# Kernel optimization log

Hardware: AMD Instinct MI355X
Metric: run time of the kernel (lower is better)

## Reference

```python
import jax, jax.numpy as jnp
import numpy as np

N_NODES = 50000
N_EDGES = 800000


def _sage_conv(h, ei, W_l, W_r, b_l):
    """PyG SAGEConv: lin_l(mean_{j->i} h_j) + lin_r(h_i). lin_l has bias, lin_r does not."""
    src, dst = ei[0], ei[1]
    # mean-aggregate raw features first (linear commutes with mean) to avoid [E, out] intermediates
    msum = jax.ops.segment_sum(h[src], dst, num_segments=N_NODES)          # [N, d]
    cnt = jax.ops.segment_sum(jnp.ones((ei.shape[1], 1), h.dtype), dst,
                              num_segments=N_NODES)                         # [N, 1]
    mean = msum / jnp.maximum(cnt, 1.0)
    return mean @ W_l + b_l + h @ W_r


def setup_inputs() -> dict:
    key = jax.random.key(0)
    ks = jax.random.split(key, 8)
    d_in, d_hid, d_out = 64, 64, 32
    return {
        "x": jax.random.normal(ks[0], (N_NODES, d_in), dtype=jnp.float32),
        "ei0": jax.random.randint(ks[1], (2, N_EDGES), 0, N_NODES, dtype=jnp.int32),
        "ei1": jax.random.randint(ks[2], (2, N_EDGES), 0, N_NODES, dtype=jnp.int32),
        "Wl": jax.random.normal(ks[3], (2, 2, d_in, d_hid), dtype=jnp.float32) * 0.05,
        "Wr": jax.random.normal(ks[4], (2, 2, d_in, d_hid), dtype=jnp.float32) * 0.05,
        "bl": jax.random.normal(ks[5], (2, 2, d_hid), dtype=jnp.float32) * 0.05,
        "lin_W": jax.random.normal(ks[6], (d_hid, d_out), dtype=jnp.float32) * 0.05,
        "lin_b": jax.random.normal(ks[7], (d_out,), dtype=jnp.float32) * 0.05,
    }


def reference(x, ei0, ei1, Wl, Wr, bl, lin_W, lin_b):
    edge_indices = (ei0, ei1)  # one edge_index per relation
    h = x
    for l in range(2):  # layers (structurally fixed)
        out = None
        for r, ei in enumerate(edge_indices):  # HeteroConv aggr='sum' over relations
            y = _sage_conv(h, ei, Wl[l, r], Wr[l, r], bl[l, r])
            out = y if out is None else out + y
        h = jax.nn.relu(out)
    return h @ lin_W + lin_b
```

## Files before the change

kernel.cpp:

```cpp
#include <hip/hip_runtime.h>

#define NN 50000
#define CAP 32
#define OVF_CAP 4096
#define SHARD_W 64
#define NSH 782
#define NPB 512

__device__ __forceinline__ unsigned short f2bf(float f) {
    unsigned u = __float_as_uint(f);
    u += 0x7fffu + ((u >> 16) & 1u);
    return (unsigned short)(u >> 16);
}
__device__ __forceinline__ float bf2f(unsigned short u) {
    return __uint_as_float(((unsigned)u) << 16);
}


__global__ __launch_bounds__(256) void shard_hist(
    const float* __restrict__ x, unsigned short* __restrict__ xb,
    const int* __restrict__ ei0, int E0,
    const int* __restrict__ ei1, int E1,
    unsigned short* __restrict__ hist16,
    int* __restrict__ ovf_cnt)
{
    int gtid = blockIdx.x * 256 + threadIdx.x;
    int gsz  = gridDim.x * 256;
    for (int i = gtid; i < NN * 16; i += gsz) {
        float4 v = ((const float4*)x)[i];
        ushort4 o;
        o.x = f2bf(v.x); o.y = f2bf(v.y); o.z = f2bf(v.z); o.w = f2bf(v.w);
        ((ushort4*)xb)[i] = o;
    }
    if (gtid < 8) ovf_cnt[gtid] = 0;

    __shared__ unsigned lh[NSH];
    int local = blockIdx.x; int rel = 0;
    if (local >= NPB) { local -= NPB; rel = 1; }
    int pb = (local & 7) * (NPB / 8) + (local >> 3);
    const int* ei = rel ? ei1 : ei0;
    int E         = rel ? E1  : E0;
    int ce = (E + NPB - 1) / NPB;
    int lo = pb * ce, hi = min(lo + ce, E);

    for (int i = threadIdx.x; i < NSH; i += 256) lh[i] = 0;
    __syncthreads();
    for (int t = lo + threadIdx.x; t < hi; t += 256)
        atomicAdd(&lh[ei[E + t] >> 6], 1u);
    __syncthreads();
    for (int i = threadIdx.x; i < NSH; i += 256)
        hist16[((size_t)rel * NSH + i) * NPB + pb] = (unsigned short)lh[i];
}

__global__ __launch_bounds__(256) void total_pass(
    const unsigned short* __restrict__ hist16, int* __restrict__ tot)
{
    int gw = (blockIdx.x * 256 + threadIdx.x) >> 6;
    int lane = threadIdx.x & 63;
    if (gw >= 2 * NSH) return;
    uint4 v = ((const uint4*)(hist16 + (size_t)gw * NPB))[lane];
    unsigned s = (v.x & 0xffffu) + (v.x >> 16) + (v.y & 0xffffu) + (v.y >> 16)
               + (v.z & 0xffffu) + (v.z >> 16) + (v.w & 0xffffu) + (v.w >> 16);
    for (int off = 32; off; off >>= 1) s += __shfl_down(s, off);
    if (lane == 0) tot[gw] = (int)s;
}

__global__ __launch_bounds__(256) void scan_pass(
    const int* __restrict__ tot, int* __restrict__ sbase)
{
    __shared__ int ps[256];
    int t = threadIdx.x;
    int v[7];
    int s = 0;
    #pragma unroll
    for (int j = 0; j < 7; j++) {
        int i = t * 7 + j;
        v[j] = (i < 2 * NSH) ? tot[i] : 0;
        s += v[j];
    }
    ps[t] = s;
    __syncthreads();
    for (int off = 1; off < 256; off <<= 1) {
        int add = (t >= off) ? ps[t - off] : 0;
        __syncthreads();
        ps[t] += add;
        __syncthreads();
    }
    int run = (t == 0) ? 0 : ps[t - 1];
    #pragma unroll
    for (int j = 0; j < 7; j++) {
        int i = t * 7 + j;
        if (i < 2 * NSH) sbase[i] = run;
        run += v[j];
    }
    if (t == 255) sbase[2 * NSH] = run;
}

__global__ __launch_bounds__(256) void blockbase_pass(
    const unsigned short* __restrict__ hist16, const int* __restrict__ sbase,
    unsigned* __restrict__ pbase)
{
    int gw = (blockIdx.x * 256 + threadIdx.x) >> 6;
    int lane = threadIdx.x & 63;
    if (gw >= 2 * NSH) return;
    uint4 v = ((const uint4*)(hist16 + (size_t)gw * NPB))[lane];
    unsigned c[8] = {v.x & 0xffffu, v.x >> 16, v.y & 0xffffu, v.y >> 16,
                     v.z & 0xffffu, v.z >> 16, v.w & 0xffffu, v.w >> 16};
    unsigned lsum = 0;
    #pragma unroll
    for (int j = 0; j < 8; j++) lsum += c[j];
    unsigned incl = lsum;
    for (int off = 1; off < 64; off <<= 1) {
        unsigned n = __shfl_up(incl, off);
        if (lane >= off) incl += n;
    }
    unsigned run = (unsigned)sbase[gw] + incl - lsum;
    unsigned* prow = pbase + (size_t)gw * NPB + lane * 8;
    #pragma unroll
    for (int j = 0; j < 8; j++) { prow[j] = run; run += c[j]; }
}

__global__ __launch_bounds__(256) void partition_pass(
    const int* __restrict__ ei0, int E0,
    const int* __restrict__ ei1, int E1,
    const unsigned* __restrict__ pbase,
    unsigned* __restrict__ compact)
{
    __shared__ unsigned lbase[NSH];
    __shared__ unsigned lrank[NSH];
    int local = blockIdx.x; int rel = 0;
    if (local >= NPB) { local -= NPB; rel = 1; }
    int pb = (local & 7) * (NPB / 8) + (local >> 3);
    const int* ei = rel ? ei1 : ei0;
    int E         = rel ? E1  : E0;
    int ce = (E + NPB - 1) / NPB;
    int lo = pb * ce, hi = min(lo + ce, E);

    for (int i = threadIdx.x; i < NSH; i += 256) {
        lbase[i] = pbase[((size_t)rel * NSH + i) * NPB + pb];
        lrank[i] = 0;
    }
    __syncthreads();
    for (int t = lo + threadIdx.x; t < hi; t += 256) {
        int dst = ei[E + t];
        int src = ei[t];
        int s = dst >> 6;
        unsigned r = atomicAdd(&lrank[s], 1u);
        compact[lbase[s] + r] = ((unsigned)dst << 16) | (unsigned)src;
    }
}

__global__ __launch_bounds__(256) void bin_pass(
    const unsigned* __restrict__ compact, const int* __restrict__ sbase,
    unsigned short* __restrict__ bins, int* __restrict__ deg,
    int2* __restrict__ ovf, int* __restrict__ ovf_cnt)
{
    __shared__ unsigned lcnt[SHARD_W];
    int bid = blockIdx.x;
    int rel = bid / NSH;
    int s   = bid - rel * NSH;
    if (threadIdx.x < SHARD_W) lcnt[threadIdx.x] = 0;
    __syncthreads();
    int base = sbase[bid];
    int tot  = sbase[bid + 1] - base;
    int taskbase = rel * NN + s * SHARD_W;
    for (int j = threadIdx.x; j < tot; j += 256) {
        unsigned e = compact[base + j];
        int dst = (int)(e >> 16);
        int src = (int)(e & 0xffffu);
        int loc = dst & (SHARD_W - 1);
        unsigned r = atomicAdd(&lcnt[loc], 1u);
        int task = taskbase + loc;
        if (r < CAP) {
            bins[(size_t)task * CAP + r] = (unsigned short)src;
        } else {
            int o = atomicAdd(ovf_cnt, 1);
            if (o < OVF_CAP) ovf[o] = make_int2(task, src);
        }
    }
    __syncthreads();
    if (threadIdx.x < SHARD_W) {
        int node = s * SHARD_W + threadIdx.x;
        if (node < NN) deg[rel * NN + node] = (int)lcnt[threadIdx.x];
    }
}

__global__ __launch_bounds__(256) void aggregate(
    const unsigned short* __restrict__ bins, const int* __restrict__ deg,
    const unsigned short* __restrict__ hb, unsigned short* __restrict__ agg,
    const int2* __restrict__ ovf, const int* __restrict__ ovf_cnt)
{
    int lane = threadIdx.x & 63;
    int half = lane >> 5;
    int p = lane & 31;
    int wid = (blockIdx.x * blockDim.x + threadIdx.x) >> 6;
    int nwaves = (gridDim.x * blockDim.x) >> 6;
    const unsigned int* hb32 = (const unsigned int*)hb;
    unsigned int* agg32 = (unsigned int*)agg;

    for (int task = wid; task < 2 * NN; task += nwaves) {
        int d = deg[task];
        int m = min(d, CAP);
        int idx = 0;
        if (lane < m) idx = bins[(size_t)task * CAP + lane];
        float a00=0.f,a01=0.f, a10=0.f,a11=0.f, a20=0.f,a21=0.f, a30=0.f,a31=0.f;
        int F = m >> 1;
        int q = 0;
        for (; q + 4 <= F; q += 4) {
            int s0 = __shfl(idx, 2*(q+0) + half);
            int s1 = __shfl(idx, 2*(q+1) + half);
            int s2 = __shfl(idx, 2*(q+2) + half);
            int s3 = __shfl(idx, 2*(q+3) + half);
            unsigned u0 = hb32[(size_t)s0 * 32 + p];
            unsigned u1 = hb32[(size_t)s1 * 32 + p];
            unsigned u2 = hb32[(size_t)s2 * 32 + p];
            unsigned u3 = hb32[(size_t)s3 * 32 + p];
            a00 += __uint_as_float(u0 << 16); a01 += __uint_as_float(u0 & 0xffff0000u);
            a10 += __uint_as_float(u1 << 16); a11 += __uint_as_float(u1 & 0xffff0000u);
            a20 += __uint_as_float(u2 << 16); a21 += __uint_as_float(u2 & 0xffff0000u);
            a30 += __uint_as_float(u3 << 16); a31 += __uint_as_float(u3 & 0xffff0000u);
        }
        for (; q < F; ++q) {
            int s = __shfl(idx, 2*q + half);
            unsigned u = hb32[(size_t)s * 32 + p];
            a00 += __uint_as_float(u << 16); a01 += __uint_as_float(u & 0xffff0000u);
        }
        if (m & 1) {
            int s = __shfl(idx, m - 1);
            if (half == 0) {
                unsigned u = hb32[(size_t)s * 32 + p];
                a00 += __uint_as_float(u << 16); a01 += __uint_as_float(u & 0xffff0000u);
            }
        }
        if (d > CAP) {
            int cnt = min(*ovf_cnt, OVF_CAP);
            for (int e = 0; e < cnt; ++e) {
                int2 v = ovf[e];
                if (v.x == task && half == 0) {
                    unsigned u = hb32[(size_t)v.y * 32 + p];
                    a00 += __uint_as_float(u << 16); a01 += __uint_as_float(u & 0xffff0000u);
                }
            }
        }
        float s0 = (a00 + a10) + (a20 + a30);
        float s1 = (a01 + a11) + (a21 + a31);
        s0 += __shfl_xor(s0, 32);
        s1 += __shfl_xor(s1, 32);
        if (half == 0) {
            float inv = 1.0f / (float)max(d, 1);
            unsigned lo = (unsigned)f2bf(s0 * inv);
            unsigned hi = (unsigned)f2bf(s1 * inv);
            agg32[(size_t)task * 32 + p] = lo | (hi << 16);
        }
    }
}

#define RST 132
__global__ __launch_bounds__(256) void layer_gemm(
    const unsigned short* __restrict__ agg0, const unsigned short* __restrict__ agg1,
    const unsigned short* __restrict__ selfb,
    const float* __restrict__ Wl0, const float* __restrict__ Wl1,
    const float* __restrict__ Wr0, const float* __restrict__ Wr1,
    const float* __restrict__ b0, const float* __restrict__ b1,
    unsigned short* __restrict__ hb16)
{
    __shared__ float Wch[64 * 64];
    __shared__ float rowsT[64 * RST];
    __shared__ float bias[64];

    int tid = threadIdx.x;
    int base = blockIdx.x * 128;
    if (tid < 64) bias[tid] = b0[tid] + b1[tid];

    int j8 = (tid & 7) * 8;
    int n4 = (tid >> 3) * 4;

    float acc[4][8];
    #pragma unroll
    for (int i = 0; i < 4; i++)
        #pragma unroll
        for (int c = 0; c < 8; c++) acc[i][c] = 0.f;

    for (int chunk = 0; chunk < 3; chunk++) {
        const float* W = (chunk == 0) ? Wl0 : (chunk == 1) ? Wl1 : Wr0;
        const unsigned short* src = (chunk == 0) ? agg0 : (chunk == 1) ? agg1 : selfb;
        __syncthreads();
        #pragma unroll
        for (int r = 0; r < 4; r++) {
            int i = tid + 256 * r;
            float4 w = *(const float4*)&W[i * 4];
            if (chunk == 2) {
                float4 w2 = *(const float4*)&Wr1[i * 4];
                w.x += w2.x; w.y += w2.y; w.z += w2.z; w.w += w2.w;
            }
            *(float4*)&Wch[i * 4] = w;
        }
        #pragma unroll
        for (int r = 0; r < 8; r++) {
            int i = tid + 256 * r;
            int node = i >> 4;
            int k4 = (i & 15) * 4;
            int g = base + node;
            ushort4 u = make_ushort4(0, 0, 0, 0);
            if (g < NN) u = *(const ushort4*)&src[(size_t)g * 64 + k4];
            rowsT[(k4 + 0) * RST + node] = bf2f(u.x);
            rowsT[(k4 + 1) * RST + node] = bf2f(u.y);
            rowsT[(k4 + 2) * RST + node] = bf2f(u.z);
            rowsT[(k4 + 3) * RST + node] = bf2f(u.w);
        }
        __syncthreads();
        #pragma unroll 4
        for (int k = 0; k < 64; k++) {
            float4 wa = *(const float4*)&Wch[k * 64 + j8];
            float4 wb = *(const float4*)&Wch[k * 64 + j8 + 4];
            float4 rv = *(const float4*)&rowsT[k * RST + n4];
            float w[8] = {wa.x, wa.y, wa.z, wa.w, wb.x, wb.y, wb.z, wb.w};
            float rr[4] = {rv.x, rv.y, rv.z, rv.w};
            #pragma unroll
            for (int i = 0; i < 4; i++)
                #pragma unroll
                for (int c = 0; c < 8; c++)
                    acc[i][c] = fmaf(rr[i], w[c], acc[i][c]);
        }
    }

    #pragma unroll
    for (int i = 0; i < 4; i++) {
        int g = base + n4 + i;
        if (g < NN) {
            ushort4 p0, p1;
            p0.x = f2bf(fmaxf(acc[i][0] + bias[j8 + 0], 0.f));
            p0.y = f2bf(fmaxf(acc[i][1] + bias[j8 + 1], 0.f));
            p0.z = f2bf(fmaxf(acc[i][2] + bias[j8 + 2], 0.f));
            p0.w = f2bf(fmaxf(acc[i][3] + bias[j8 + 3], 0.f));
            p1.x = f2bf(fmaxf(acc[i][4] + bias[j8 + 4], 0.f));
            p1.y = f2bf(fmaxf(acc[i][5] + bias[j8 + 5], 0.f));
            p1.z = f2bf(fmaxf(acc[i][6] + bias[j8 + 6], 0.f));
            p1.w = f2bf(fmaxf(acc[i][7] + bias[j8 + 7], 0.f));
            *(ushort4*)&hb16[(size_t)g * 64 + j8]     = p0;
            *(ushort4*)&hb16[(size_t)g * 64 + j8 + 4] = p1;
        }
    }
}

__global__ __launch_bounds__(256) void layer_gemm_final(
    const unsigned short* __restrict__ agg0, const unsigned short* __restrict__ agg1,
    const unsigned short* __restrict__ selfb,
    const float* __restrict__ Wl0, const float* __restrict__ Wl1,
    const float* __restrict__ Wr0, const float* __restrict__ Wr1,
    const float* __restrict__ b0, const float* __restrict__ b1,
    const float* __restrict__ linW, const float* __restrict__ linb,
    float* __restrict__ out)
{
    __shared__ float Wch[64 * 64];
    __shared__ float rowsT[64 * RST];
    __shared__ float bias[64];

    int tid = threadIdx.x;
    int base = blockIdx.x * 128;
    if (tid < 64) bias[tid] = b0[tid] + b1[tid];

    int j8 = (tid & 7) * 8;
    int n4 = (tid >> 3) * 4;

    float acc[4][8];
    #pragma unroll
    for (int i = 0; i < 4; i++)
        #pragma unroll
        for (int c = 0; c < 8; c++) acc[i][c] = 0.f;

    for (int chunk = 0; chunk < 3; chunk++) {
        const float* W = (chunk == 0) ? Wl0 : (chunk == 1) ? Wl1 : Wr0;
        const unsigned short* src = (chunk == 0) ? agg0 : (chunk == 1) ? agg1 : selfb;
        __syncthreads();
        #pragma unroll
        for (int r = 0; r < 4; r++) {
            int i = tid + 256 * r;
            float4 w = *(const float4*)&W[i * 4];
            if (chunk == 2) {
                float4 w2 = *(const float4*)&Wr1[i * 4];
                w.x += w2.x; w.y += w2.y; w.z += w2.z; w.w += w2.w;
            }
            *(float4*)&Wch[i * 4] = w;
        }
        #pragma unroll
        for (int r = 0; r < 8; r++) {
            int i = tid + 256 * r;
            int node = i >> 4;
            int k4 = (i & 15) * 4;
            int g = base + node;
            ushort4 u = make_ushort4(0, 0, 0, 0);
            if (g < NN) u = *(const ushort4*)&src[(size_t)g * 64 + k4];
            rowsT[(k4 + 0) * RST + node] = bf2f(u.x);
            rowsT[(k4 + 1) * RST + node] = bf2f(u.y);
            rowsT[(k4 + 2) * RST + node] = bf2f(u.z);
            rowsT[(k4 + 3) * RST + node] = bf2f(u.w);
        }
        __syncthreads();
        #pragma unroll 4
        for (int k = 0; k < 64; k++) {
            float4 wa = *(const float4*)&Wch[k * 64 + j8];
            float4 wb = *(const float4*)&Wch[k * 64 + j8 + 4];
            float4 rv = *(const float4*)&rowsT[k * RST + n4];
            float w[8] = {wa.x, wa.y, wa.z, wa.w, wb.x, wb.y, wb.z, wb.w};
            float rr[4] = {rv.x, rv.y, rv.z, rv.w};
            #pragma unroll
            for (int i = 0; i < 4; i++)
                #pragma unroll
                for (int c = 0; c < 8; c++)
                    acc[i][c] = fmaf(rr[i], w[c], acc[i][c]);
        }
    }

    float o[4][8];
    #pragma unroll
    for (int i = 0; i < 4; i++)
        #pragma unroll
        for (int c = 0; c < 8; c++)
            o[i][c] = fmaxf(acc[i][c] + bias[j8 + c], 0.f);

    __syncthreads();

    #pragma unroll
    for (int r = 0; r < 2; r++) {
        int i = tid + 256 * r;
        *(float4*)&Wch[i * 4] = *(const float4*)&linW[i * 4];
    }
    if (tid < 32) bias[tid] = linb[tid];
    #pragma unroll
    for (int i = 0; i < 4; i++)
        #pragma unroll
        for (int c = 0; c < 8; c++)
            rowsT[(j8 + c) * RST + (n4 + i)] = o[i][c];
    __syncthreads();

    int j4 = (tid & 7) * 4;
    float acc2[4][4];
    #pragma unroll
    for (int i = 0; i < 4; i++)
        #pragma unroll
        for (int c = 0; c < 4; c++) acc2[i][c] = 0.f;
    #pragma unroll 4
    for (int k = 0; k < 64; k++) {
        float4 w = *(const float4*)&Wch[k * 32 + j4];
        float4 rv = *(const float4*)&rowsT[k * RST + n4];
        float wr[4] = {w.x, w.y, w.z, w.w};
        float rr[4] = {rv.x, rv.y, rv.z, rv.w};
        #pragma unroll
        for (int i = 0; i < 4; i++)
            #pragma unroll
            for (int c = 0; c < 4; c++)
                acc2[i][c] = fmaf(rr[i], wr[c], acc2[i][c]);
    }
    #pragma unroll
    for (int i = 0; i < 4; i++) {
        int g = base + n4 + i;
        if (g < NN) {
            float4 ov;
            ov.x = acc2[i][0] + bias[j4 + 0];
            ov.y = acc2[i][1] + bias[j4 + 1];
            ov.z = acc2[i][2] + bias[j4 + 2];
            ov.w = acc2[i][3] + bias[j4 + 3];
            *(float4*)&out[(size_t)g * 32 + j4] = ov;
        }
    }
}

extern "C" void kernel_launch(void* const* d_in, const int* in_sizes, int n_in,
                              void* d_out, int out_size, void* d_ws, size_t ws_size,
                              hipStream_t stream)
{
    const float* x    = (const float*)d_in[0];
    const int*   ei0  = (const int*)d_in[1];
    const int*   ei1  = (const int*)d_in[2];
    const float* Wl   = (const float*)d_in[3];
    const float* Wr   = (const float*)d_in[4];
    const float* bl   = (const float*)d_in[5];
    const float* linW = (const float*)d_in[6];
    const float* linb = (const float*)d_in[7];
    float* out = (float*)d_out;

    int E0 = in_sizes[1] / 2;
    int E1 = in_sizes[2] / 2;

    unsigned short* bins = (unsigned short*)d_ws;
    unsigned short* h1b  = bins + (size_t)2 * NN * CAP;
    unsigned short* aggb = h1b + (size_t)NN * 64;
    unsigned short* agg0 = aggb;
    unsigned short* agg1 = aggb + (size_t)NN * 64;
    unsigned short* xb   = aggb + (size_t)2 * NN * 64;
    int*  deg     = (int*)(xb + (size_t)NN * 64);
    int*  ovf_cnt = deg + 2 * NN;
    int2* ovf     = (int2*)(ovf_cnt + 8);

    unsigned*       compact = (unsigned*)h1b;
    unsigned short* hist16  = aggb;
    unsigned*       pbase   = (unsigned*)(aggb + (size_t)2 * NSH * NPB);
    int*            tot     = (int*)(aggb + (size_t)2 * NSH * NPB * 3);
    int*            sbase   = tot + 2 * NSH;

    dim3 blk(256);
    int ggrid = (NN + 127) / 128;
    int wave_grid = (2 * NSH * 64 + 255) / 256;

    shard_hist<<<2 * NPB, blk, 0, stream>>>(x, xb, ei0, E0, ei1, E1,
                                            hist16, ovf_cnt);
    total_pass<<<wave_grid, blk, 0, stream>>>(hist16, tot);
    scan_pass<<<1, blk, 0, stream>>>(tot, sbase);
    blockbase_pass<<<wave_grid, blk, 0, stream>>>(hist16, sbase, pbase);
    partition_pass<<<2 * NPB, blk, 0, stream>>>(ei0, E0, ei1, E1, pbase, compact);
    bin_pass<<<2 * NSH, blk, 0, stream>>>(compact, sbase, bins, deg, ovf, ovf_cnt);

    aggregate<<<4096, blk, 0, stream>>>(bins, deg, xb, aggb, ovf, ovf_cnt);
    layer_gemm<<<ggrid, blk, 0, stream>>>(agg0, agg1, xb,
        Wl + 0, Wl + 4096, Wr + 0, Wr + 4096, bl + 0, bl + 64, h1b);

    aggregate<<<4096, blk, 0, stream>>>(bins, deg, h1b, aggb, ovf, ovf_cnt);
    layer_gemm_final<<<ggrid, blk, 0, stream>>>(agg0, agg1, h1b,
        Wl + 8192, Wl + 12288, Wr + 8192, Wr + 12288, bl + 128, bl + 192,
        linW, linb, out);
}
```

Baseline: 243.6 us.

## Fuse edge binning into per-shard aggregation using LDS bins

Removes the separate bin_pass kernel and the global bins, deg and overflow arrays. Each aggregation block now bins its shard's compacted edges into shared memory, keeping overflow edges in a local list, then gathers neighbour features for its 64 nodes. This avoids writing and re-reading the global bin arrays and saves a launch. In exchange, binning runs once per layer instead of once overall, and the aggregate grid is fixed at one block per shard, with each wave handling 16 nodes in sequence.

```diff
diff --git a/kernel.cpp b/kernel.cpp
--- a/kernel.cpp
+++ b/kernel.cpp
@@ -2,7 +2,7 @@
 
 #define NN 50000
 #define CAP 32
-#define OVF_CAP 4096
+#define OVF_LDS 1024
 #define SHARD_W 64
 #define NSH 782
 #define NPB 512
@@ -21,8 +21,7 @@
     const float* __restrict__ x, unsigned short* __restrict__ xb,
     const int* __restrict__ ei0, int E0,
     const int* __restrict__ ei1, int E1,
-    unsigned short* __restrict__ hist16,
-    int* __restrict__ ovf_cnt)
+    unsigned short* __restrict__ hist16)
 {
     int gtid = blockIdx.x * 256 + threadIdx.x;
     int gsz  = gridDim.x * 256;
@@ -32,7 +31,6 @@
         o.x = f2bf(v.x); o.y = f2bf(v.y); o.z = f2bf(v.z); o.w = f2bf(v.w);
         ((ushort4*)xb)[i] = o;
     }
-    if (gtid < 8) ovf_cnt[gtid] = 0;
 
     __shared__ unsigned lh[NSH];
     int local = blockIdx.x; int rel = 0;
@@ -150,59 +148,51 @@
     }
 }
 
-__global__ __launch_bounds__(256) void bin_pass(
+__global__ __launch_bounds__(256) void aggregate_shard(
     const unsigned* __restrict__ compact, const int* __restrict__ sbase,
-    unsigned short* __restrict__ bins, int* __restrict__ deg,
-    int2* __restrict__ ovf, int* __restrict__ ovf_cnt)
-{
+    const unsigned short* __restrict__ hb, unsigned short* __restrict__ agg)
+{
+    __shared__ unsigned short lbins[SHARD_W * CAP];
     __shared__ unsigned lcnt[SHARD_W];
+    __shared__ unsigned lovf[OVF_LDS];
+    __shared__ unsigned lovf_cnt;
+
     int bid = blockIdx.x;
     int rel = bid / NSH;
     int s   = bid - rel * NSH;
-    if (threadIdx.x < SHARD_W) lcnt[threadIdx.x] = 0;
-    __syncthreads();
-    int base = sbase[bid];
-    int tot  = sbase[bid + 1] - base;
-    int taskbase = rel * NN + s * SHARD_W;
-    for (int j = threadIdx.x; j < tot; j += 256) {
-        unsigned e = compact[base + j];
-        int dst = (int)(e >> 16);
-        int src = (int)(e & 0xffffu);
-        int loc = dst & (SHARD_W - 1);
-        unsigned r = atomicAdd(&lcnt[loc], 1u);
-        int task = taskbase + loc;
-        if (r < CAP) {
-            bins[(size_t)task * CAP + r] = (unsigned short)src;
-        } else {
-            int o = atomicAdd(ovf_cnt, 1);
-            if (o < OVF_CAP) ovf[o] = make_int2(task, src);
-        }
-    }
-    __syncthreads();
-    if (threadIdx.x < SHARD_W) {
-        int node = s * SHARD_W + threadIdx.x;
-        if (node < NN) deg[rel * NN + node] = (int)lcnt[threadIdx.x];
-    }
-}
-
-__global__ __launch_bounds__(256) void aggregate(
-    const unsigned short* __restrict__ bins, const int* __restrict__ deg,
-    const unsigned short* __restrict__ hb, unsigned short* __restrict__ agg,
-    const int2* __restrict__ ovf, const int* __restrict__ ovf_cnt)
-{
-    int lane = threadIdx.x & 63;
+    int tid = threadIdx.x;
+    int lane = tid & 63;
     int half = lane >> 5;
     int p = lane & 31;
-    int wid = (blockIdx.x * blockDim.x + threadIdx.x) >> 6;
-    int nwaves = (gridDim.x * blockDim.x) >> 6;
-    const unsigned int* hb32 = (const unsigned int*)hb;
-    unsigned int* agg32 = (unsigned int*)agg;
-
-    for (int task = wid; task < 2 * NN; task += nwaves) {
-        int d = deg[task];
+    int wid = tid >> 6;
+
+    if (tid < SHARD_W) lcnt[tid] = 0;
+    if (tid == 0) lovf_cnt = 0;
+    __syncthreads();
+
+    int base = sbase[bid];
+    int tt   = sbase[bid + 1] - base;
+    for (int j = tid; j < tt; j += 256) {
+        unsigned e = compact[base + j];
+        int loc = (int)(e >> 16) & (SHARD_W - 1);
+        unsigned r = atomicAdd(&lcnt[loc], 1u);
+        if (r < CAP) {
+            lbins[loc * CAP + r] = (unsigned short)(e & 0xffffu);
+        } else {
+            unsigned o = atomicAdd(&lovf_cnt, 1u);
+            if (o < OVF_LDS) lovf[o] = ((unsigned)loc << 16) | (e & 0xffffu);
+        }
+    }
+    __syncthreads();
+
+    const unsigned* hb32 = (const unsigned*)hb;
+    unsigned* agg32 = (unsigned*)agg;
+    for (int t = 0; t < 16; ++t) {
+        int loc = wid * 16 + t;
+        int d = (int)lcnt[loc];
         int m = min(d, CAP);
         int idx = 0;
-        if (lane < m) idx = bins[(size_t)task * CAP + lane];
+        if (lane < m) idx = lbins[loc * CAP + lane];
         float a00=0.f,a01=0.f, a10=0.f,a11=0.f, a20=0.f,a21=0.f, a30=0.f,a31=0.f;
         int F = m >> 1;
         int q = 0;
@@ -221,23 +211,23 @@
             a30 += __uint_as_float(u3 << 16); a31 += __uint_as_float(u3 & 0xffff0000u);
         }
         for (; q < F; ++q) {
-            int s = __shfl(idx, 2*q + half);
-            unsigned u = hb32[(size_t)s * 32 + p];
+            int s0 = __shfl(idx, 2*q + half);
+            unsigned u = hb32[(size_t)s0 * 32 + p];
             a00 += __uint_as_float(u << 16); a01 += __uint_as_float(u & 0xffff0000u);
         }
         if (m & 1) {
-            int s = __shfl(idx, m - 1);
+            int s0 = __shfl(idx, m - 1);
             if (half == 0) {
-                unsigned u = hb32[(size_t)s * 32 + p];
+                unsigned u = hb32[(size_t)s0 * 32 + p];
                 a00 += __uint_as_float(u << 16); a01 += __uint_as_float(u & 0xffff0000u);
             }
         }
         if (d > CAP) {
-            int cnt = min(*ovf_cnt, OVF_CAP);
-            for (int e = 0; e < cnt; ++e) {
-                int2 v = ovf[e];
-                if (v.x == task && half == 0) {
-                    unsigned u = hb32[(size_t)v.y * 32 + p];
+            int cnt = min((int)lovf_cnt, OVF_LDS);
+            for (int e0 = 0; e0 < cnt; ++e0) {
+                unsigned v = lovf[e0];
+                if ((int)(v >> 16) == loc && half == 0) {
+                    unsigned u = hb32[(size_t)(v & 0xffffu) * 32 + p];
                     a00 += __uint_as_float(u << 16); a01 += __uint_as_float(u & 0xffff0000u);
                 }
             }
@@ -246,11 +236,12 @@
         float s1 = (a01 + a11) + (a21 + a31);
         s0 += __shfl_xor(s0, 32);
         s1 += __shfl_xor(s1, 32);
-        if (half == 0) {
+        int node = s * SHARD_W + loc;
+        if (half == 0 && node < NN) {
             float inv = 1.0f / (float)max(d, 1);
             unsigned lo = (unsigned)f2bf(s0 * inv);
             unsigned hi = (unsigned)f2bf(s1 * inv);
-            agg32[(size_t)task * 32 + p] = lo | (hi << 16);
+            agg32[((size_t)rel * NN + node) * 32 + p] = lo | (hi << 16);
         }
     }
 }
@@ -483,39 +474,33 @@
     int E0 = in_sizes[1] / 2;
     int E1 = in_sizes[2] / 2;
 
-    unsigned short* bins = (unsigned short*)d_ws;
-    unsigned short* h1b  = bins + (size_t)2 * NN * CAP;
+    unsigned*       compact = (unsigned*)d_ws;
+    unsigned short* h1b  = (unsigned short*)d_ws + (size_t)2 * NN * CAP;
     unsigned short* aggb = h1b + (size_t)NN * 64;
     unsigned short* agg0 = aggb;
     unsigned short* agg1 = aggb + (size_t)NN * 64;
     unsigned short* xb   = aggb + (size_t)2 * NN * 64;
-    int*  deg     = (int*)(xb + (size_t)NN * 64);
-    int*  ovf_cnt = deg + 2 * NN;
-    int2* ovf     = (int2*)(ovf_cnt + 8);
-
-    unsigned*       compact = (unsigned*)h1b;
-    unsigned short* hist16  = aggb;
-    unsigned*       pbase   = (unsigned*)(aggb + (size_t)2 * NSH * NPB);
-    int*            tot     = (int*)(aggb + (size_t)2 * NSH * NPB * 3);
-    int*            sbase   = tot + 2 * NSH;
+    int*            tot   = (int*)(xb + (size_t)NN * 64);
+    int*            sbase = tot + 2 * NSH;
+
+    unsigned short* hist16 = aggb;
+    unsigned*       pbase  = (unsigned*)(aggb + (size_t)2 * NSH * NPB);
 
     dim3 blk(256);
     int ggrid = (NN + 127) / 128;
     int wave_grid = (2 * NSH * 64 + 255) / 256;
 
-    shard_hist<<<2 * NPB, blk, 0, stream>>>(x, xb, ei0, E0, ei1, E1,
-                                            hist16, ovf_cnt);
+    shard_hist<<<2 * NPB, blk, 0, stream>>>(x, xb, ei0, E0, ei1, E1, hist16);
     total_pass<<<wave_grid, blk, 0, stream>>>(hist16, tot);
     scan_pass<<<1, blk, 0, stream>>>(tot, sbase);
     blockbase_pass<<<wave_grid, blk, 0, stream>>>(hist16, sbase, pbase);
     partition_pass<<<2 * NPB, blk, 0, stream>>>(ei0, E0, ei1, E1, pbase, compact);
-    bin_pass<<<2 * NSH, blk, 0, stream>>>(compact, sbase, bins, deg, ovf, ovf_cnt);
-
-    aggregate<<<4096, blk, 0, stream>>>(bins, deg, xb, aggb, ovf, ovf_cnt);
+
+    aggregate_shard<<<2 * NSH, blk, 0, stream>>>(compact, sbase, xb, aggb);
     layer_gemm<<<ggrid, blk, 0, stream>>>(agg0, agg1, xb,
         Wl + 0, Wl + 4096, Wr + 0, Wr + 4096, bl + 0, bl + 64, h1b);
 
-    aggregate<<<4096, blk, 0, stream>>>(bins, deg, h1b, aggb, ovf, ovf_cnt);
+    aggregate_shard<<<2 * NSH, blk, 0, stream>>>(compact, sbase, h1b, aggb);
     layer_gemm_final<<<ggrid, blk, 0, stream>>>(agg0, agg1, h1b,
         Wl + 8192, Wl + 12288, Wr + 8192, Wr + 12288, bl + 128, bl + 192,
         linW, linb, out);
```

After: 241.9 us. About the same (-0.7%).
